# Optimization experiments

Hardware: AMD Instinct MI355X
Metric: run time of the kernel (lower is better)

## Reference

```python
import jax, jax.numpy as jnp
import numpy as np
from jax import lax

T, H, W, HID, K = 128, 128, 128, 32, 3
DN = ('NCDHW', 'OIDHW', 'NCDHW')


def conv3dc(x, w, b=None, squeeze=False):
    # Conv3dC: 3D conv, kernel KxKxK, 'SAME' padding; return_squeezed drops channel dim
    y = lax.conv_general_dilated(x, w, (1, 1, 1), 'SAME', dimension_numbers=DN)
    if b is not None:
        y = y + b.reshape(1, -1, 1, 1, 1)
    if squeeze:
        y = jnp.squeeze(y, 1)
    return y


def setup_inputs() -> dict:
    key = jax.random.key(0)
    ks = jax.random.split(key, 10)
    X = jax.random.normal(ks[0], (1, T, H, W), dtype=jnp.float32)
    U = jax.random.normal(ks[1], (H * W, 1), dtype=jnp.float32) * 0.01
    V = jax.random.normal(ks[2], (1, T), dtype=jnp.float32) * 0.01
    M = jax.random.uniform(ks[3], (1, 1, T, H, W), dtype=jnp.float32)
    convM_w = jax.random.normal(ks[4], (HID, 1, K, K, K), dtype=jnp.float32) * 0.05
    conv0_w = jax.random.normal(ks[5], (1, HID, K, K, K), dtype=jnp.float32) * 0.05
    conv0_b = jnp.zeros((1,), dtype=jnp.float32)
    conv1_w = jax.random.normal(ks[6], (1, HID, K, K, K), dtype=jnp.float32) * 0.05
    conv2_w = jax.random.normal(ks[7], (HID, 1, K, K, K), dtype=jnp.float32) * 0.05
    conv4_w = jax.random.normal(ks[8], (1, HID, K, K, K), dtype=jnp.float32) * 0.05
    return {
        'X': X, 'U': U, 'V': V, 'M': M,
        'convM_w': convM_w, 'conv0_w': conv0_w, 'conv0_b': conv0_b,
        'conv1_w': conv1_w, 'conv2_w': conv2_w, 'conv4_w': conv4_w,
        'tau_s_raw': jnp.float32(1.0),
        'mask_scaling': jnp.float32(5.0),
        'g': jnp.ones((HID,), dtype=jnp.float32),
        'th': jnp.full((128,), 1.8, dtype=jnp.float32),
        'g2': jnp.ones((H,), dtype=jnp.float32),
        'u_learn2': jnp.ones((5,), dtype=jnp.float32),
        'v_learn2': jnp.ones((5,), dtype=jnp.float32),
    }


def reference(X, U, V, M, convM_w, conv0_w, conv0_b, conv1_w, conv2_w, conv4_w,
              tau_s_raw, mask_scaling, g, th, g2, u_learn2, v_learn2):
    tau_s = jax.nn.softplus(tau_s_raw)
    B, Td, Hd, Wd = X.shape
    Mh = conv3dc(M, convM_w)                                       # [1,HID,T,H,W]
    bg = 1.0 - jax.nn.relu(conv3dc(Mh, conv0_w, conv0_b, squeeze=True))  # [1,T,H,W]
    bg2 = jnp.square(bg)
    # 5-step unrolled rank-1 U/V gradient descent (faithful, incl. raw .view on (HW,T))
    for i in range(5):
        temp = bg2 * (X - jnp.reshape(U @ V, (1, Td, Hd, Wd)))
        temp = temp.reshape(Td, Hd * Wd)
        grad_U = temp.T @ V.T                                      # [HW,1]
        U = U + 1e-05 * u_learn2[i] * grad_U
        grad_V = (temp @ U).reshape(1, Td)                         # [1,T]
        V = V + 1e-05 * v_learn2[i] * grad_V
    L = (U @ V).T.reshape(Td, Hd, Wd)[None]                        # [1,T,H,W]
    fg2 = jnp.square(X - L)
    _X = tau_s * conv3dc((1.0 - conv3dc(Mh, conv1_w)) * fg2[:, None], conv2_w)
    Mtmp = Mh + _X                                                 # [1,HID,T,H,W]
    # soft_l1_reweighted2
    z = Mtmp.reshape(1, HID, Td, Hd * Wd)
    th2 = (th[None, None, :] * g2[None, :, None] * g[:, None, None]).reshape(HID, Hd * Wd)
    z = jnp.sign(z) * jax.nn.relu(jnp.abs(z) - th2[None, :, None, :])
    Mtmp = z.reshape(1, HID, Td, Hd, Wd)
    Mtmp = conv3dc(Mtmp, conv4_w, squeeze=True)                    # [1,T,H,W]
    M_out = jax.nn.sigmoid((Mtmp - 0.5) * mask_scaling)
    return (X, U, V, M_out)
```

## Files before the change

### kernel.cpp

```cpp
#include <hip/hip_runtime.h>
#include <math.h>

#define Tn 128
#define Hn 128
#define Wn 128
#define Cn 32
#define NVOX (Tn*Hn*Wn)

typedef float4 f4;
typedef unsigned short ushort_t;
typedef __attribute__((ext_vector_type(8))) short short8;
typedef __attribute__((ext_vector_type(4))) float f32x4;
typedef __attribute__((ext_vector_type(2))) float f32x2;

__device__ __forceinline__ unsigned bfpack2(float a, float b) {
  unsigned ua = __float_as_uint(a), ub = __float_as_uint(b);
  ua = (ua + 0x7FFFu + ((ua >> 16) & 1u)) >> 16;
  ub = (ub + 0x7FFFu + ((ub >> 16) & 1u)) >> 16;
  return ua | (ub << 16);
}
__device__ __forceinline__ unsigned short bf1(float a) {
  unsigned u = __float_as_uint(a);
  u = (u + 0x7FFFu + ((u >> 16) & 1u)) >> 16;
  return (unsigned short)u;
}
__device__ __forceinline__ float bflo(unsigned p) { return __uint_as_float(p << 16); }
__device__ __forceinline__ float bfhi(unsigned p) { return __uint_as_float(p & 0xFFFF0000u); }
__device__ __forceinline__ float bfs(unsigned short s) { return __uint_as_float((unsigned)s << 16); }

__device__ __forceinline__ f32x2 pfma(f32x2 a, float b, f32x2 c) {
  f32x2 bb = {b, b};
  return __builtin_elementwise_fma(a, bb, c);
}

union U4S8 { uint4 u; short8 s; };


__global__ __launch_bounds__(256) void k_convM(
    const float* __restrict__ M, const float* __restrict__ wM,
    uint4* __restrict__ Mh, const float* __restrict__ X,
    f4* __restrict__ outX)
{
  __shared__ float sm[1224];
  const int w0 = blockIdx.x*32, h0 = blockIdx.y*4, t0 = blockIdx.z*4;
  const int tid = threadIdx.x;
  const bool interior = (w0 != 0) && (w0 != 96) && (h0 != 0) && (h0 != 124)
                     && (t0 != 0) && (t0 != 124);
  for (int idx = tid; idx < 1224; idx += 256) {
    int lw = idx % 34, r = idx / 34, lh = r % 6, ld = r / 6;
    int gw = w0 - 1 + lw, gh = h0 - 1 + lh, gt = t0 - 1 + ld;
    float v = 0.f;
    if (interior || ((unsigned)gw < Wn && (unsigned)gh < Hn && (unsigned)gt < Tn))
      v = M[((long)gt*Hn + gh)*Wn + gw];
    sm[idx] = v;
  }
  const int bid = (blockIdx.z*32 + blockIdx.y)*4 + blockIdx.x;
  if (tid < 128) outX[bid*128 + tid] = ((const f4*)X)[bid*128 + tid];
  __syncthreads();

  const int wp = tid & 15, th = (tid>>4)&3, td = tid>>6;
  f32x2 m2[27];
  #pragma unroll
  for (int kd = 0; kd < 3; ++kd)
    #pragma unroll
    for (int kh = 0; kh < 3; ++kh) {
      const float* row = &sm[(((td+kd)*6) + (th+kh))*34 + wp];
      int k0 = (kd*3 + kh)*3;
      m2[k0+0] = (f32x2){row[0], row[16]};
      m2[k0+1] = (f32x2){row[1], row[17]};
      m2[k0+2] = (f32x2){row[2], row[18]};
    }
  const long voxA = ((long)(t0+td)*Hn + (h0+th))*Wn + (w0+wp);
  #pragma unroll
  for (int j = 0; j < 4; ++j) {
    float rA[8], rB[8];
    #pragma unroll
    for (int e = 0; e < 8; ++e) {
      const int c = 8*j + e;
      f32x2 acc = {0.f, 0.f};
      #pragma unroll
      for (int k = 0; k < 27; ++k)
        acc = pfma(m2[k], wM[c*27 + k], acc);
      rA[e] = acc.x; rB[e] = acc.y;
    }
    uint4 oA, oB;
    oA.x = bfpack2(rA[0],rA[1]); oA.y = bfpack2(rA[2],rA[3]);
    oA.z = bfpack2(rA[4],rA[5]); oA.w = bfpack2(rA[6],rA[7]);
    oB.x = bfpack2(rB[0],rB[1]); oB.y = bfpack2(rB[2],rB[3]);
    oB.z = bfpack2(rB[4],rB[5]); oB.w = bfpack2(rB[6],rB[7]);
    Mh[(size_t)j*NVOX + voxA]      = oA;
    Mh[(size_t)j*NVOX + voxA + 16] = oB;
  }
}

template<int S>
__device__ __forceinline__ auto& sel3(f32x4 (&a0)[4], f32x4 (&a1)[4], f32x4 (&a2)[4]) {
  if constexpr (S == 0) return a0;
  else if constexpr (S == 1) return a1;
  else return a2;
}

template<int P>
__device__ __forceinline__ void load_plane(
    const uint4* __restrict__ SRC, int tbase, int h0, int w0v, long lofs,
    int n, bool wL, bool wR, U4S8 (&A)[6][3])
{
  const int gt = tbase - 1 + P;
  const bool tok = (unsigned)gt < Tn;
  #pragma unroll
  for (int hr = 0; hr < 6; ++hr) {
    const int gh = h0 - 1 + hr;
    if (tok && (unsigned)gh < Hn) {
      const uint4* rowp = SRC + lofs + (((long)gt*Hn + gh)*Wn + (w0v - 1));
      A[hr][0].u = rowp[0];
      A[hr][1].u = rowp[1];
      A[hr][2].u = rowp[2];
    } else {
      A[hr][0].u = (uint4){0u,0u,0u,0u};
      A[hr][1].u = (uint4){0u,0u,0u,0u};
      A[hr][2].u = (uint4){0u,0u,0u,0u};
    }
  }
  if (wL && n == 0) {
    #pragma unroll
    for (int hr = 0; hr < 6; ++hr) A[hr][0].u = (uint4){0u,0u,0u,0u};
  }
  if (wR && n == 15) {
    #pragma unroll
    for (int hr = 0; hr < 6; ++hr) A[hr][2].u = (uint4){0u,0u,0u,0u};
  }
}

template<int KD>
__device__ __forceinline__ void kd_taps(
    const U4S8 (&A)[6][3], const uint4* sB, int bbase, int bstep,
    f32x4 (&acc)[4])
{
  const f32x4 fz = {0.f,0.f,0.f,0.f};
  #pragma unroll
  for (int kh = 0; kh < 3; ++kh)
    #pragma unroll
    for (int kw = 0; kw < 3; ++kw) {
      const int tap = KD*9 + kh*3 + kw;
      U4S8 b; b.u = sB[tap*bstep + bbase];
      const bool first = (KD == 0) && (kh == 0) && (kw == 0);
      #pragma unroll
      for (int lh = 0; lh < 4; ++lh)
        acc[lh] = __builtin_amdgcn_mfma_f32_16x16x32_bf16(
            A[lh+kh][kw].s, b.s, first ? fz : acc[lh], 0, 0, 0);
    }
}

template<int MODE, int P>
__device__ __forceinline__ void mfma_retire(
    const uint4* sB, const U4S8 (&A)[6][3],
    int tbase, int h0, int w0v, int bbase, int bstep,
    int n, int kg, float scal,
    ushort_t* __restrict__ outH, float* __restrict__ outF,
    f32x4 (&a0)[4], f32x4 (&a1)[4], f32x4 (&a2)[4])
{
  constexpr int kdlo = (P > 7) ? (P - 7) : 0;
  constexpr int kdhi = (P < 2) ? P : 2;
  if constexpr (0 >= kdlo && 0 <= kdhi)
    kd_taps<0>(A, sB, bbase, bstep, sel3<(P - 0) % 3>(a0, a1, a2));
  if constexpr (1 >= kdlo && 1 <= kdhi)
    kd_taps<1>(A, sB, bbase, bstep, sel3<(P - 1) % 3>(a0, a1, a2));
  if constexpr (2 >= kdlo && 2 <= kdhi)
    kd_taps<2>(A, sB, bbase, bstep, sel3<(P - 2) % 3>(a0, a1, a2));

  if constexpr (P >= 2) {
    constexpr int TR = P - 2;
    f32x4 (&acc)[4] = sel3<TR % 3>(a0, a1, a2);
    const int tt = tbase + TR;
    if constexpr (MODE == 0) {
      if (n < 2) {
        #pragma unroll
        for (int lh = 0; lh < 4; ++lh) {
          const long vbase = ((long)tt*Hn + (h0+lh))*Wn + w0v + kg*4;
          #pragma unroll
          for (int r = 0; r < 4; ++r) {
            float y = acc[lh][r];
            if (n == 0) { float bg = 1.f - fmaxf(y + scal, 0.f); outH[vbase+r] = bf1(bg*bg); }
            else        { outF[vbase+r] = 1.f - y; }
          }
        }
      }
    } else {
      if (n == 0) {
        #pragma unroll
        for (int lh = 0; lh < 4; ++lh) {
          const long vbase = ((long)tt*Hn + (h0+lh))*Wn + w0v + kg*4;
          #pragma unroll
          for (int r = 0; r < 4; ++r) {
            float y = (acc[lh][r] - 0.5f)*scal;
            outF[vbase+r] = 1.f/(1.f + expf(-y));
          }
        }
      }
    }
  }
}

template<int MODE>
__global__ __launch_bounds__(256, 2) void k_conv_fused(
    const uint4* __restrict__ SRC, const float* __restrict__ wAp,
    const float* __restrict__ wBp, const float* __restrict__ bias_or_ms,
    ushort_t* __restrict__ outH, float* __restrict__ outF)
{
  __shared__ uint4 sB[MODE == 0 ? 220 : 112];
  const int tid = threadIdx.x;
  const int lane = tid & 63;
  const int n = lane & 15, kg = lane >> 4;

  if constexpr (MODE == 0) {
    for (int idx = tid; idx < 220; idx += 256) {
      uint4 v = {0u,0u,0u,0u};
      if (idx < 216) {
        int tap = idx >> 3, col = (idx >> 2) & 1, kgi = idx & 3;
        const float* wp = col ? wBp : wAp;
        v.x = bfpack2(wp[(kgi*8+0)*27+tap], wp[(kgi*8+1)*27+tap]);
        v.y = bfpack2(wp[(kgi*8+2)*27+tap], wp[(kgi*8+3)*27+tap]);
        v.z = bfpack2(wp[(kgi*8+4)*27+tap], wp[(kgi*8+5)*27+tap]);
        v.w = bfpack2(wp[(kgi*8+6)*27+tap], wp[(kgi*8+7)*27+tap]);
      }
      sB[idx] = v;
    }
  } else {
    for (int idx = tid; idx < 112; idx += 256) {
      uint4 v = {0u,0u,0u,0u};
      if (idx < 108) {
        int tap = idx >> 2, kgi = idx & 3;
        v.x = bfpack2(wAp[(kgi*8+0)*27+tap], wAp[(kgi*8+1)*27+tap]);
        v.y = bfpack2(wAp[(kgi*8+2)*27+tap], wAp[(kgi*8+3)*27+tap]);
        v.z = bfpack2(wAp[(kgi*8+4)*27+tap], wAp[(kgi*8+5)*27+tap]);
        v.w = bfpack2(wAp[(kgi*8+6)*27+tap], wAp[(kgi*8+7)*27+tap]);
      }
      sB[idx] = v;
    }
  }
  const float scal = bias_or_ms[0];
  const int bbase = (MODE == 0) ? ((n < 2) ? (n*4 + kg) : (216 + kg))
                                : ((n == 0) ? kg : (108 + kg));
  const int bstep = (MODE == 0) ? ((n < 2) ? 8 : 0) : ((n == 0) ? 4 : 0);

  const int w0v = blockIdx.x*16, h0 = blockIdx.y*4;
  const int wv = __builtin_amdgcn_readfirstlane(tid >> 6);
  const int tbase = (blockIdx.z*4 + wv)*8;
  const long lofs = (long)kg*NVOX + n;
  const bool wL = (w0v == 0), wR = (w0v == Wn-16);
  __syncthreads();

  f32x4 a0[4], a1[4], a2[4];
  U4S8 Aa[6][3], Ab[6][3];

  #define PL(P, AR) load_plane<P>(SRC, tbase, h0, w0v, lofs, n, wL, wR, AR);
  #define PM(P, AR) mfma_retire<MODE,P>(sB, AR, tbase, h0, w0v, bbase, bstep, \
                                        n, kg, scal, outH, outF, a0, a1, a2);
  #define SB __builtin_amdgcn_sched_barrier(0);

  PL(0, Aa) PL(1, Ab) SB
  PM(0, Aa) PL(2, Aa) SB
  PM(1, Ab) PL(3, Ab) SB
  PM(2, Aa) PL(4, Aa) SB
  PM(3, Ab) PL(5, Ab) SB
  PM(4, Aa) PL(6, Aa) SB
  PM(5, Ab) PL(7, Ab) SB
  PM(6, Aa) PL(8, Aa) SB
  PM(7, Ab) PL(9, Ab) SB
  PM(8, Aa) SB
  PM(9, Ab)

  #undef PL
  #undef PM
  #undef SB
}

__global__ __launch_bounds__(512) void k_G(
    const float* __restrict__ X, const ushort_t* __restrict__ bg2h,
    const float* __restrict__ U0, const float* __restrict__ V0,
    float* __restrict__ G)
{
  __shared__ float Vs[128], Ucol[128], red[512];
  const int h = blockIdx.x;
  const int tid = threadIdx.x;
  const int w = tid & 127, tq = tid >> 7;
  if (tid < 128) Vs[tid] = V0[tid];
  else if (tid < 256) Ucol[tid-128] = U0[(tid-128)*128 + h];
  __syncthreads();
  const float vw = Vs[w];
  float acc = 0.f;
  const int tstart = tq*32;
  for (int t = tstart; t < tstart+32; ++t) {
    int idx = (t*Hn + h)*Wn + w;
    acc += bfs(bg2h[idx])*(X[idx] - Ucol[t]*vw)*Vs[t];
  }
  red[tid] = acc;
  __syncthreads();
  if (tq == 0)
    G[h*128 + w] = red[w] + red[128+w] + red[256+w] + red[384+w];
}

__global__ __launch_bounds__(256) void k_dotT(
    const float* __restrict__ X, const ushort_t* __restrict__ bg2h,
    const float* __restrict__ U0, const float* __restrict__ V0,
    const float* __restrict__ D, float* __restrict__ out)
{
  __shared__ float Uc[128], Vs[128], red[256];
  const int t = blockIdx.x, tid = threadIdx.x;
  if (tid < 128) { Uc[tid] = U0[t*128 + tid]; Vs[tid] = V0[tid]; }
  __syncthreads();
  float acc = 0.f;
  for (int idx = tid; idx < 16384; idx += 256) {
    int h = idx >> 7, w = idx & 127;
    int gi = t*16384 + idx;
    acc += bfs(bg2h[gi])*(X[gi] - Uc[h]*Vs[w])*D[idx];
  }
  red[tid] = acc;
  __syncthreads();
  for (int s = 128; s > 0; s >>= 1) {
    if (tid < s) red[tid] += red[tid+s];
    __syncthreads();
  }
  if (tid == 0) out[t] = red[0];
}

__global__ __launch_bounds__(256) void k_final(
    const float* __restrict__ U0, const float* __restrict__ V0,
    const float* __restrict__ G, const float* __restrict__ u1,
    const float* __restrict__ g2, const float* __restrict__ ul,
    const float* __restrict__ vl,
    float* __restrict__ Ua, float* __restrict__ Va,
    float* __restrict__ outU, float* __restrict__ outV)
{
  const int tid = threadIdx.x;
  float A = 0.f, cu1 = 0.f, cg2 = 0.f;
  #pragma unroll
  for (int i = 0; i < 5; ++i) {
    float ai = 1e-5f*ul[i], bi = 1e-5f*vl[i];
    A += ai; cu1 += bi; cg2 += bi*A;
  }
  for (int idx = tid; idx < 16384; idx += 256) {
    float u = U0[idx] + A*G[idx];
    Ua[idx] = u; outU[idx] = u;
  }
  if (tid < 128) {
    float v = V0[tid] + cu1*u1[tid] + cg2*g2[tid];
    Va[tid] = v; outV[tid] = v;
  }
}

__global__ __launch_bounds__(256) void k_z(
    const float* __restrict__ X, const float* __restrict__ c1m,
    const float* __restrict__ Uf, const float* __restrict__ Vf,
    const float* __restrict__ w2, uint4* __restrict__ Mh,
    const float* __restrict__ taup, const float* __restrict__ g,
    const float* __restrict__ g2, const float* __restrict__ th)
{
  __shared__ float sm[1224];
  const int w0 = blockIdx.x*32, h0 = blockIdx.y*4, t0 = blockIdx.z*4;
  const int tid = threadIdx.x;
  const bool interior = (w0 != 0) && (w0 != 96) && (h0 != 0) && (h0 != 124)
                     && (t0 != 0) && (t0 != 124);
  for (int idx = tid; idx < 1224; idx += 256) {
    int lw = idx % 34, r = idx / 34, lh = r % 6, ld = r / 6;
    int gw = w0 - 1 + lw, gh = h0 - 1 + lh, gt = t0 - 1 + ld;
    float qv = 0.f;
    if (interior || ((unsigned)gw < Wn && (unsigned)gh < Hn && (unsigned)gt < Tn)) {
      long gi = ((long)gt*Hn + gh)*Wn + gw;
      float d = X[gi] - Uf[gh*Wn + gw]*Vf[gt];
      qv = c1m[gi]*d*d;
    }
    sm[idx] = qv;
  }
  __syncthreads();

  const float tau_s = log1pf(expf(taup[0]));
  const int wp = tid & 15, thl = (tid>>4)&3, td = tid>>6;
  f32x2 m2[27];
  #pragma unroll
  for (int kd = 0; kd < 3; ++kd)
    #pragma unroll
    for (int kh = 0; kh < 3; ++kh) {
      const float* row = &sm[(((td+kd)*6) + (thl+kh))*34 + wp];
      int k0 = (kd*3 + kh)*3;
      m2[k0+0] = (f32x2){row[0], row[16]};
      m2[k0+1] = (f32x2){row[1], row[17]};
      m2[k0+2] = (f32x2){row[2], row[18]};
    }
  const int h = h0 + thl, wA = w0 + wp;
  const long voxA = ((long)(t0+td)*Hn + h)*Wn + wA;
  const float g2h = g2[h];
  const float thwA = g2h*th[wA], thwB = g2h*th[wA+16];

  #define ZJ(J)                                                             \
  {                                                                         \
    uint4 pA = Mh[(size_t)(J)*NVOX + voxA];                                 \
    uint4 pB = Mh[(size_t)(J)*NVOX + voxA + 16];                            \
    f32x2 in2[8] = {                                                        \
      {bflo(pA.x), bflo(pB.x)}, {bfhi(pA.x), bfhi(pB.x)},                   \
      {bflo(pA.y), bflo(pB.y)}, {bfhi(pA.y), bfhi(pB.y)},                   \
      {bflo(pA.z), bflo(pB.z)}, {bfhi(pA.z), bfhi(pB.z)},                   \
      {bflo(pA.w), bflo(pB.w)}, {bfhi(pA.w), bfhi(pB.w)}};                  \
    float oA[8], oB[8];                                                     \
    _Pragma("unroll")                                                       \
    for (int e = 0; e < 8; ++e) {                                           \
      const int c = 8*(J) + e;                                              \
      f32x2 acc = {0.f, 0.f};                                               \
      _Pragma("unroll")                                                     \
      for (int k = 0; k < 27; ++k)                                          \
        acc = pfma(m2[k], w2[c*27 + k], acc);                               \
      f32x2 rr = pfma(acc, tau_s, in2[e]);                                  \
      float gc = g[c];                                                      \
      float aA = fabsf(rr.x) - gc*thwA;                                     \
      float aB = fabsf(rr.y) - gc*thwB;                                     \
      oA[e] = (aA > 0.f) ? copysignf(aA, rr.x) : 0.f;                       \
      oB[e] = (aB > 0.f) ? copysignf(aB, rr.y) : 0.f;                       \
    }                                                                       \
    uint4 qA, qB;                                                           \
    qA.x = bfpack2(oA[0],oA[1]); qA.y = bfpack2(oA[2],oA[3]);               \
    qA.z = bfpack2(oA[4],oA[5]); qA.w = bfpack2(oA[6],oA[7]);               \
    qB.x = bfpack2(oB[0],oB[1]); qB.y = bfpack2(oB[2],oB[3]);               \
    qB.z = bfpack2(oB[4],oB[5]); qB.w = bfpack2(oB[6],oB[7]);               \
    Mh[(size_t)(J)*NVOX + voxA]      = qA;                                  \
    Mh[(size_t)(J)*NVOX + voxA + 16] = qB;                                  \
  }

  ZJ(0)
  ZJ(1)
  ZJ(2)
  ZJ(3)
  #undef ZJ
}

extern "C" void kernel_launch(void* const* d_in, const int* in_sizes, int n_in,
                              void* d_out, int out_size, void* d_ws, size_t ws_size,
                              hipStream_t stream)
{
  const float* X   = (const float*)d_in[0];
  const float* U0  = (const float*)d_in[1];
  const float* V0  = (const float*)d_in[2];
  const float* M   = (const float*)d_in[3];
  const float* wM  = (const float*)d_in[4];
  const float* w0  = (const float*)d_in[5];
  const float* b0  = (const float*)d_in[6];
  const float* w1  = (const float*)d_in[7];
  const float* w2  = (const float*)d_in[8];
  const float* w4  = (const float*)d_in[9];
  const float* tau = (const float*)d_in[10];
  const float* ms  = (const float*)d_in[11];
  const float* g   = (const float*)d_in[12];
  const float* th  = (const float*)d_in[13];
  const float* g2  = (const float*)d_in[14];
  const float* ul  = (const float*)d_in[15];
  const float* vl  = (const float*)d_in[16];

  float*    c1m  = (float*)d_ws;
  uint4*    Mh   = (uint4*)((char*)d_ws + (size_t)NVOX*4);
  ushort_t* bg2h = (ushort_t*)((char*)Mh + (size_t)NVOX*64);
  float*    Ua   = (float*)((char*)bg2h + (size_t)NVOX*2);
  float*    Va   = Ua + 16384;
  float*    G    = Va + 128;
  float*    u1   = G + 16384;
  float*    g2v  = u1 + 128;

  float* out_f  = (float*)d_out;
  f4*    outX   = (f4*)d_out;
  float* outU   = out_f + NVOX;
  float* outV   = outU + 16384;
  float* outM   = outV + 128;

  k_convM <<<dim3(4,32,32), 256, 0, stream>>>(M, wM, Mh, X, outX);
  k_conv_fused<0><<<dim3(8,32,4), 256, 0, stream>>>(Mh, w0, w1, b0, bg2h, c1m);

  k_G    <<<128, 512, 0, stream>>>(X, bg2h, U0, V0, G);
  k_dotT <<<128, 256, 0, stream>>>(X, bg2h, U0, V0, U0, u1);
  k_dotT <<<128, 256, 0, stream>>>(X, bg2h, U0, V0, G, g2v);
  k_final<<<1, 256, 0, stream>>>(U0, V0, G, u1, g2v, ul, vl, Ua, Va, outU, outV);

  k_z    <<<dim3(4,32,32), 256, 0, stream>>>(X, c1m, Ua, Va, w2, Mh,
                                             tau, g, g2, th);
  k_conv_fused<1><<<dim3(8,32,4), 256, 0, stream>>>(Mh, w4, w4, ms, nullptr, outM);
}
```

Measured before the change: 392.5 us.

## Map depth-time outputs onto MFMA columns to use one accumulator set

Restructures the fused 32->1 channel conv kernel so that the MFMA N dimension (16 columns) carries different output time steps (and, in mode 0, both conv outputs) instead of mostly zero-padded columns. Weights are re-laid out per (conv, kd) so each lane selects its kd tap row from the plane index, letting one accumulator set cover all 8 output time steps across 10 input planes. This removes the three rotating accumulator arrays and the double-buffered A registers, and launch bounds are raised to allow more waves per CU. Epilogue stores become vectorised uint2/float4 writes done once at the end. In exchange, the explicit load/compute double-buffer overlap is dropped and the schedule relies on occupancy to hide memory latency.

```diff
diff --git a/kernel.cpp b/kernel.cpp
--- a/kernel.cpp
+++ b/kernel.cpp
@@ -93,20 +93,15 @@
   }
 }
 
-template<int S>
-__device__ __forceinline__ auto& sel3(f32x4 (&a0)[4], f32x4 (&a1)[4], f32x4 (&a2)[4]) {
-  if constexpr (S == 0) return a0;
-  else if constexpr (S == 1) return a1;
-  else return a2;
-}
-
-template<int P>
-__device__ __forceinline__ void load_plane(
-    const uint4* __restrict__ SRC, int tbase, int h0, int w0v, long lofs,
-    int n, bool wL, bool wR, U4S8 (&A)[6][3])
+template<int MODE, int P>
+__device__ __forceinline__ void plane_step(
+    const uint4* __restrict__ SRC, const uint4* sBw,
+    int tbase, int h0, int w0v, long lofs,
+    int n, int kg, bool wL, bool wR, f32x4 (&acc)[4])
 {
   const int gt = tbase - 1 + P;
   const bool tok = (unsigned)gt < Tn;
+  U4S8 A[6][3];
   #pragma unroll
   for (int hr = 0; hr < 6; ++hr) {
     const int gh = h0 - 1 + hr;
@@ -129,120 +124,69 @@
     #pragma unroll
     for (int hr = 0; hr < 6; ++hr) A[hr][2].u = (uint4){0u,0u,0u,0u};
   }
-}
-
-template<int KD>
-__device__ __forceinline__ void kd_taps(
-    const U4S8 (&A)[6][3], const uint4* sB, int bbase, int bstep,
-    f32x4 (&acc)[4])
-{
+  __builtin_amdgcn_sched_barrier(0);
+
+  const int kdl = P - (n & 7);
+  int base;
+  if constexpr (MODE == 0) {
+    const int cv = n >> 3;
+    base = ((unsigned)kdl <= 2u) ? ((cv*3 + kdl)*36 + kg) : (216 + kg);
+  } else {
+    base = (((unsigned)kdl <= 2u) && (n < 8)) ? (kdl*36 + kg) : (108 + kg);
+  }
   const f32x4 fz = {0.f,0.f,0.f,0.f};
   #pragma unroll
-  for (int kh = 0; kh < 3; ++kh)
-    #pragma unroll
-    for (int kw = 0; kw < 3; ++kw) {
-      const int tap = KD*9 + kh*3 + kw;
-      U4S8 b; b.u = sB[tap*bstep + bbase];
-      const bool first = (KD == 0) && (kh == 0) && (kw == 0);
-      #pragma unroll
-      for (int lh = 0; lh < 4; ++lh)
-        acc[lh] = __builtin_amdgcn_mfma_f32_16x16x32_bf16(
-            A[lh+kh][kw].s, b.s, first ? fz : acc[lh], 0, 0, 0);
-    }
-}
-
-template<int MODE, int P>
-__device__ __forceinline__ void mfma_retire(
-    const uint4* sB, const U4S8 (&A)[6][3],
-    int tbase, int h0, int w0v, int bbase, int bstep,
-    int n, int kg, float scal,
-    ushort_t* __restrict__ outH, float* __restrict__ outF,
-    f32x4 (&a0)[4], f32x4 (&a1)[4], f32x4 (&a2)[4])
-{
-  constexpr int kdlo = (P > 7) ? (P - 7) : 0;
-  constexpr int kdhi = (P < 2) ? P : 2;
-  if constexpr (0 >= kdlo && 0 <= kdhi)
-    kd_taps<0>(A, sB, bbase, bstep, sel3<(P - 0) % 3>(a0, a1, a2));
-  if constexpr (1 >= kdlo && 1 <= kdhi)
-    kd_taps<1>(A, sB, bbase, bstep, sel3<(P - 1) % 3>(a0, a1, a2));
-  if constexpr (2 >= kdlo && 2 <= kdhi)
-    kd_taps<2>(A, sB, bbase, bstep, sel3<(P - 2) % 3>(a0, a1, a2));
-
-  if constexpr (P >= 2) {
-    constexpr int TR = P - 2;
-    f32x4 (&acc)[4] = sel3<TR % 3>(a0, a1, a2);
-    const int tt = tbase + TR;
-    if constexpr (MODE == 0) {
-      if (n < 2) {
-        #pragma unroll
-        for (int lh = 0; lh < 4; ++lh) {
-          const long vbase = ((long)tt*Hn + (h0+lh))*Wn + w0v + kg*4;
-          #pragma unroll
-          for (int r = 0; r < 4; ++r) {
-            float y = acc[lh][r];
-            if (n == 0) { float bg = 1.f - fmaxf(y + scal, 0.f); outH[vbase+r] = bf1(bg*bg); }
-            else        { outF[vbase+r] = 1.f - y; }
-          }
-        }
-      }
-    } else {
-      if (n == 0) {
-        #pragma unroll
-        for (int lh = 0; lh < 4; ++lh) {
-          const long vbase = ((long)tt*Hn + (h0+lh))*Wn + w0v + kg*4;
-          #pragma unroll
-          for (int r = 0; r < 4; ++r) {
-            float y = (acc[lh][r] - 0.5f)*scal;
-            outF[vbase+r] = 1.f/(1.f + expf(-y));
-          }
-        }
-      }
-    }
+  for (int t9 = 0; t9 < 9; ++t9) {
+    const int kh = t9 / 3, kw = t9 % 3;
+    U4S8 b; b.u = sBw[base + t9*4];
+    const bool first = (P == 0 && t9 == 0);
+    #pragma unroll
+    for (int lh = 0; lh < 4; ++lh)
+      acc[lh] = __builtin_amdgcn_mfma_f32_16x16x32_bf16(
+          A[lh+kh][kw].s, b.s, first ? fz : acc[lh], 0, 0, 0);
   }
 }
 
 template<int MODE>
-__global__ __launch_bounds__(256, 2) void k_conv_fused(
+__global__ __launch_bounds__(256, 4) void k_conv_fused(
     const uint4* __restrict__ SRC, const float* __restrict__ wAp,
     const float* __restrict__ wBp, const float* __restrict__ bias_or_ms,
     ushort_t* __restrict__ outH, float* __restrict__ outF)
 {
-  __shared__ uint4 sB[MODE == 0 ? 220 : 112];
+  __shared__ uint4 sBw[MODE == 0 ? 252 : 144];
   const int tid = threadIdx.x;
   const int lane = tid & 63;
   const int n = lane & 15, kg = lane >> 4;
 
   if constexpr (MODE == 0) {
-    for (int idx = tid; idx < 220; idx += 256) {
+    for (int idx = tid; idx < 252; idx += 256) {
       uint4 v = {0u,0u,0u,0u};
       if (idx < 216) {
-        int tap = idx >> 3, col = (idx >> 2) & 1, kgi = idx & 3;
-        const float* wp = col ? wBp : wAp;
+        int ckd = idx / 36, rem = idx % 36, t9 = rem >> 2, kgi = rem & 3;
+        int conv = ckd / 3, kd = ckd % 3, tap = kd*9 + t9;
+        const float* wp = conv ? wBp : wAp;
         v.x = bfpack2(wp[(kgi*8+0)*27+tap], wp[(kgi*8+1)*27+tap]);
         v.y = bfpack2(wp[(kgi*8+2)*27+tap], wp[(kgi*8+3)*27+tap]);
         v.z = bfpack2(wp[(kgi*8+4)*27+tap], wp[(kgi*8+5)*27+tap]);
         v.w = bfpack2(wp[(kgi*8+6)*27+tap], wp[(kgi*8+7)*27+tap]);
       }
-      sB[idx] = v;
+      sBw[idx] = v;
     }
   } else {
-    for (int idx = tid; idx < 112; idx += 256) {
+    for (int idx = tid; idx < 144; idx += 256) {
       uint4 v = {0u,0u,0u,0u};
       if (idx < 108) {
-        int tap = idx >> 2, kgi = idx & 3;
+        int kd = idx / 36, rem = idx % 36, t9 = rem >> 2, kgi = rem & 3;
+        int tap = kd*9 + t9;
         v.x = bfpack2(wAp[(kgi*8+0)*27+tap], wAp[(kgi*8+1)*27+tap]);
         v.y = bfpack2(wAp[(kgi*8+2)*27+tap], wAp[(kgi*8+3)*27+tap]);
         v.z = bfpack2(wAp[(kgi*8+4)*27+tap], wAp[(kgi*8+5)*27+tap]);
         v.w = bfpack2(wAp[(kgi*8+6)*27+tap], wAp[(kgi*8+7)*27+tap]);
       }
-      sB[idx] = v;
+      sBw[idx] = v;
     }
   }
   const float scal = bias_or_ms[0];
-  const int bbase = (MODE == 0) ? ((n < 2) ? (n*4 + kg) : (216 + kg))
-                                : ((n == 0) ? kg : (108 + kg));
-  const int bstep = (MODE == 0) ? ((n < 2) ? 8 : 0) : ((n == 0) ? 4 : 0);
-
   const int w0v = blockIdx.x*16, h0 = blockIdx.y*4;
   const int wv = __builtin_amdgcn_readfirstlane(tid >> 6);
   const int tbase = (blockIdx.z*4 + wv)*8;
@@ -250,29 +194,52 @@
   const bool wL = (w0v == 0), wR = (w0v == Wn-16);
   __syncthreads();
 
-  f32x4 a0[4], a1[4], a2[4];
-  U4S8 Aa[6][3], Ab[6][3];
-
-  #define PL(P, AR) load_plane<P>(SRC, tbase, h0, w0v, lofs, n, wL, wR, AR);
-  #define PM(P, AR) mfma_retire<MODE,P>(sB, AR, tbase, h0, w0v, bbase, bstep, \
-                                        n, kg, scal, outH, outF, a0, a1, a2);
-  #define SB __builtin_amdgcn_sched_barrier(0);
-
-  PL(0, Aa) PL(1, Ab) SB
-  PM(0, Aa) PL(2, Aa) SB
-  PM(1, Ab) PL(3, Ab) SB
-  PM(2, Aa) PL(4, Aa) SB
-  PM(3, Ab) PL(5, Ab) SB
-  PM(4, Aa) PL(6, Aa) SB
-  PM(5, Ab) PL(7, Ab) SB
-  PM(6, Aa) PL(8, Aa) SB
-  PM(7, Ab) PL(9, Ab) SB
-  PM(8, Aa) SB
-  PM(9, Ab)
-
-  #undef PL
-  #undef PM
-  #undef SB
+  f32x4 acc[4];
+  #define PS(P) plane_step<MODE,P>(SRC, sBw, tbase, h0, w0v, lofs, n, kg, wL, wR, acc);
+  PS(0) PS(1) PS(2) PS(3) PS(4) PS(5) PS(6) PS(7) PS(8) PS(9)
+  #undef PS
+
+  const int tq = n & 7;
+  const int tt = tbase + tq;
+  if constexpr (MODE == 0) {
+    if (n < 8) {
+      #pragma unroll
+      for (int lh = 0; lh < 4; ++lh) {
+        const long vb = ((long)tt*Hn + (h0+lh))*Wn + w0v + kg*4;
+        float q[4];
+        #pragma unroll
+        for (int r = 0; r < 4; ++r) {
+          float bg = 1.f - fmaxf(acc[lh][r] + scal, 0.f);
+          q[r] = bg*bg;
+        }
+        uint2 pk; pk.x = bfpack2(q[0],q[1]); pk.y = bfpack2(q[2],q[3]);
+        *(uint2*)&outH[vb] = pk;
+      }
+    } else {
+      #pragma unroll
+      for (int lh = 0; lh < 4; ++lh) {
+        const long vb = ((long)tt*Hn + (h0+lh))*Wn + w0v + kg*4;
+        f4 o;
+        o.x = 1.f - acc[lh][0]; o.y = 1.f - acc[lh][1];
+        o.z = 1.f - acc[lh][2]; o.w = 1.f - acc[lh][3];
+        *(f4*)&outF[vb] = o;
+      }
+    }
+  } else {
+    if (n < 8) {
+      #pragma unroll
+      for (int lh = 0; lh < 4; ++lh) {
+        const long vb = ((long)tt*Hn + (h0+lh))*Wn + w0v + kg*4;
+        f4 o;
+        #pragma unroll
+        for (int r = 0; r < 4; ++r) {
+          float y = (acc[lh][r] - 0.5f)*scal;
+          ((float*)&o)[r] = 1.f/(1.f + expf(-y));
+        }
+        *(f4*)&outF[vb] = o;
+      }
+    }
+  }
 }
 
 __global__ __launch_bounds__(512) void k_G(
```

After: 362.8 us. 7.6% less time.
